# Kernel optimization log

Measured on AMD Instinct MI355X. Metric: run time of the kernel, lower is better.

Reference implementation:

```python
import jax, jax.numpy as jnp
import numpy as np

K = 50          # NEC paper uses p=50 neighbors
DELTA = 1e-3    # kernel smoothing constant


def setup_inputs() -> dict:
    key = jax.random.key(0)
    ks = jax.random.split(key, 8)
    B, D_IN, D, A, C = 512, 2, 128, 3, 200000
    s = lambda fan_in: 1.0 / np.sqrt(fan_in)
    return {
        "x": jax.random.normal(ks[0], (B, D_IN), jnp.float32),
        "W1": jax.random.normal(ks[1], (D_IN, D), jnp.float32) * s(D_IN),
        "b1": jnp.zeros((D,), jnp.float32),
        "W2": jax.random.normal(ks[2], (D, D), jnp.float32) * s(D),
        "b2": jnp.zeros((D,), jnp.float32),
        "W3": jax.random.normal(ks[3], (D, D), jnp.float32) * s(D),
        "b3": jnp.zeros((D,), jnp.float32),
        "W4": jax.random.normal(ks[4], (D, D), jnp.float32) * s(D),
        "b4": jnp.zeros((D,), jnp.float32),
        "keys": jax.random.normal(ks[5], (A, C, D), jnp.float32),
        "mem_values": jax.random.normal(ks[6], (A, C), jnp.float32),
    }


def _encode(x, W1, b1, W2, b2, W3, b3, W4, b4):
    h = jax.nn.relu(x @ W1 + b1)
    h = jax.nn.relu(h @ W2 + b2)
    h = jax.nn.relu(h @ W3 + b3)
    return h @ W4 + b4  # [B, D]


def _dnd_lookup(h, keys, mem_values):
    # h: [B, D]; keys: [A, C, D]; mem_values: [A, C]
    q2 = jnp.sum(h * h, axis=-1)                       # [B]
    k2 = jnp.sum(keys * keys, axis=-1)                 # [A, C]
    cross = jnp.einsum("bd,acd->bac", h, keys)         # [B, A, C]
    d2 = jnp.maximum(q2[:, None, None] + k2[None] - 2.0 * cross, 0.0)
    neg_d, idx = jax.lax.top_k(-d2, K)                  # [B, A, K]
    d_top = -neg_d
    w = 1.0 / (d_top + DELTA)                           # NEC kernel
    w = w / jnp.sum(w, axis=-1, keepdims=True)
    a_idx = jnp.arange(keys.shape[0])[None, :, None]    # [1, A, 1]
    v_top = mem_values[a_idx, idx]                      # gather -> [B, A, K]
    values = jnp.sum(w * v_top, axis=-1)                # [B, A]
    return values


def reference(x, W1, b1, W2, b2, W3, b3, W4, b4, keys, mem_values):
    h = _encode(x, W1, b1, W2, b2, W3, b3, W4, b4)
    values = _dnd_lookup(h, keys, mem_values)
    actions = jnp.argmax(values, axis=-1)
    return values, actions
```

## Files before the change

kernel.cpp:

```cpp
#include <hip/hip_runtime.h>
#include <hip/hip_bf16.h>
#include <math.h>

#define B_    512
#define DIM   128
#define A_    3
#define C_    200000
#define K_    50
#define DELTA 1e-3

typedef __attribute__((ext_vector_type(8))) short bf16x8;
typedef __attribute__((ext_vector_type(4))) float f32x4;

#define NBIN_A 128
#define CAP_A  1024
#define ROWCH  12500

#define NBLK4  250
#define GT4    32
#define GTPB4  25

#define AOFF_H64   0u
#define AOFF_H32   524288u
#define AOFF_HBF   786432u
#define AOFF_Q2    917504u
#define AOFF_V64   1718272u
#define AOFF_BINS  8022016u
#define NEED_A     (8022016ull + 307200000ull)

#define NBIN_B 192
#define CAP_B  768
#define BM_B   64
#define BN_B   128
#define TPC_B  16
#define CHUNK_B (TPC_B*BN_B)
#define NCH_B  ((C_ + CHUNK_B - 1)/CHUNK_B)

#define BOFF_H32   0u
#define BOFF_H64   262144u
#define BOFF_Q2    786432u
#define BOFF_K2    788480u
#define BOFF_HIST  3188480u
#define BOFF_TAU   4368128u
#define BOFF_CNT   4374272u
#define BOFF_V64   4380416u
#define BOFF_CAND  4392704u

static __device__ inline unsigned short f2bf(float x) {
    union { float f; unsigned u; } c; c.f = x;
    unsigned r = (c.u + 0x7FFFu + ((c.u >> 16) & 1u)) >> 16;
    return (unsigned short)r;
}
static __device__ inline unsigned pkbf(float a, float b) {
    __hip_bfloat162 t = __float22bfloat162_rn(make_float2(a, b));
    union { __hip_bfloat162 h; unsigned u; } cv; cv.h = t; return cv.u;
}

__global__ __launch_bounds__(128) void mlp_kernel(
    const float* __restrict__ x,
    const float* __restrict__ W1, const float* __restrict__ b1,
    const float* __restrict__ W2, const float* __restrict__ b2,
    const float* __restrict__ W3, const float* __restrict__ b3,
    const float* __restrict__ W4, const float* __restrict__ b4,
    float* __restrict__ h32, unsigned short* __restrict__ hbf,
    double* __restrict__ h64, float* __restrict__ q2)
{
    int b = blockIdx.x, t = threadIdx.x;
    __shared__ double s0[DIM], s1[DIM];
    double x0 = (double)x[b*2+0], x1 = (double)x[b*2+1];
    double h = x0*(double)W1[t] + x1*(double)W1[DIM+t] + (double)b1[t];
    s0[t] = h > 0.0 ? h : 0.0;
    __syncthreads();
    double acc = (double)b2[t];
    for (int k = 0; k < DIM; k++) acc += s0[k]*(double)W2[k*DIM+t];
    s1[t] = acc > 0.0 ? acc : 0.0;
    __syncthreads();
    acc = (double)b3[t];
    for (int k = 0; k < DIM; k++) acc += s1[k]*(double)W3[k*DIM+t];
    s0[t] = acc > 0.0 ? acc : 0.0;
    __syncthreads();
    acc = (double)b4[t];
    for (int k = 0; k < DIM; k++) acc += s0[k]*(double)W4[k*DIM+t];
    h64[b*DIM+t] = acc;
    float hf = (float)acc;
    h32[b*DIM+t] = hf;
    hbf[b*DIM+t] = f2bf(hf);
    s1[t] = acc*acc;
    __syncthreads();
    for (int s = 64; s > 0; s >>= 1) { if (t < s) s1[t] += s1[t+s]; __syncthreads(); }
    if (t == 0) q2[b] = (float)s1[0];
}

static __device__ inline void load2(float4 lv[2], const float* __restrict__ ka,
                                    int nrow, int hh) {
    const float4* gp = (const float4*)(ka + (size_t)nrow*DIM) + hh*2;
    lv[0] = gp[0]; lv[1] = gp[1];
}
static __device__ inline void conv_store32(const float4 lv[2], char* sBn,
                                           float* k2n, int r, int hh) {
    float4 v0 = lv[0], v1 = lv[1];
    float ss = v0.x*v0.x + v0.y*v0.y + v0.z*v0.z + v0.w*v0.w
             + v1.x*v1.x + v1.y*v1.y + v1.z*v1.z + v1.w*v1.w;
    int4 pk;
    pk.x = (int)pkbf(v0.x, v0.y); pk.y = (int)pkbf(v0.z, v0.w);
    pk.z = (int)pkbf(v1.x, v1.y); pk.w = (int)pkbf(v1.z, v1.w);
    *(int4*)(sBn + r*256 + ((hh ^ (r & 7)) << 4)) = pk;
    ss += __shfl_xor(ss, 1, 64);
    ss += __shfl_xor(ss, 2, 64);
    ss += __shfl_xor(ss, 4, 64);
    ss += __shfl_xor(ss, 8, 64);
    if (hh == 0) k2n[r] = ss;
}

__global__ __launch_bounds__(512, 1) void gemm4_kernel(
    const float* __restrict__ keys, const unsigned short* __restrict__ hbf,
    const float* __restrict__ q2, unsigned char* __restrict__ bins)
{
    const int blk = blockIdx.x, a = blockIdx.y;
    const int tid = threadIdx.x;
    const int lane = tid & 63, w = tid >> 6;
    const int lm = lane & 15, kh = lane >> 4;

    __shared__ __align__(16) short sA[512*128];
    __shared__ __align__(16) short sB[2][32*128];
    __shared__ float q2s[512];
    __shared__ float k2s[2][32];

    #pragma unroll
    for (int u = 0; u < 16; u++) {
        int idx = u*512 + tid;
        int rr = idx >> 4, cc = idx & 15;
        int4 gv = ((const int4*)hbf)[rr*16 + cc];
        *(int4*)((char*)sA + rr*256 + ((cc ^ (rr & 7)) << 4)) = gv;
    }
    q2s[tid] = q2[tid];

    const int r = tid >> 4, hh = tid & 15;
    const float* ka = keys + (size_t)a*C_*DIM;
    const int nbase = blk*(GT4*GTPB4);

    float4 lv[2];
    load2(lv, ka, nbase + r, hh);
    conv_store32(lv, (char*)&sB[0][0], k2s[0], r, hh);
    __syncthreads();

    unsigned char* rp0; unsigned char* rp1; unsigned char* rp2; unsigned char* rp3;
    {
        unsigned char* base = bins + (size_t)(a*B_)*C_ + kh*4;
        rp0 = base + (size_t)(w*64 +  0 + lm)*C_;
        rp1 = base + (size_t)(w*64 + 16 + lm)*C_;
        rp2 = base + (size_t)(w*64 + 32 + lm)*C_;
        rp3 = base + (size_t)(w*64 + 48 + lm)*C_;
    }

    unsigned pkp[8];
    #pragma unroll
    for (int u = 0; u < 8; u++) pkp[u] = 0;
    int n0_prev = 0;

    int cur = 0;
    for (int t = 0; t < GTPB4; t++) {
        const int n0 = nbase + t*GT4;
        const bool more = (t + 1 < GTPB4);

        if (more) load2(lv, ka, n0 + GT4 + r, hh);
        if (t > 0) {
            *(unsigned*)(rp0 + n0_prev     ) = pkp[0];
            *(unsigned*)(rp0 + n0_prev + 16) = pkp[1];
            *(unsigned*)(rp1 + n0_prev     ) = pkp[2];
            *(unsigned*)(rp1 + n0_prev + 16) = pkp[3];
            *(unsigned*)(rp2 + n0_prev     ) = pkp[4];
            *(unsigned*)(rp2 + n0_prev + 16) = pkp[5];
            *(unsigned*)(rp3 + n0_prev     ) = pkp[6];
            *(unsigned*)(rp3 + n0_prev + 16) = pkp[7];
        }

        f32x4 acc[2][4];
        #pragma unroll
        for (int i = 0; i < 2; i++)
            #pragma unroll
            for (int j = 0; j < 4; j++) acc[i][j] = (f32x4){0.f, 0.f, 0.f, 0.f};

        const char* sBc = (const char*)&sB[cur][0];
        #pragma unroll
        for (int kst = 0; kst < 4; kst++) {
            bf16x8 af[2], bfv[4];
            #pragma unroll
            for (int i = 0; i < 2; i++) {
                int nr = i*16 + lm;
                af[i] = *(const bf16x8*)(sBc + nr*256 + ((((kst<<2) + kh) ^ (nr & 7)) << 4));
            }
            #pragma unroll
            for (int j = 0; j < 4; j++) {
                int br = w*64 + j*16 + lm;
                bfv[j] = *(const bf16x8*)((const char*)sA + br*256 + ((((kst<<2) + kh) ^ (br & 7)) << 4));
            }
            #pragma unroll
            for (int i = 0; i < 2; i++)
                #pragma unroll
                for (int j = 0; j < 4; j++)
                    acc[i][j] = __builtin_amdgcn_mfma_f32_16x16x32_bf16(af[i], bfv[j], acc[i][j], 0, 0, 0);
        }

        {
            float4 kq0 = *(const float4*)&k2s[cur][kh*4];
            float4 kq1 = *(const float4*)&k2s[cur][16 + kh*4];
            #pragma unroll
            for (int j = 0; j < 4; j++) {
                float q2v = q2s[w*64 + j*16 + lm];
                #pragma unroll
                for (int i = 0; i < 2; i++) {
                    float4 kq = (i == 0) ? kq0 : kq1;
                    unsigned pk = 0;
                    #pragma unroll
                    for (int rg = 0; rg < 4; rg++) {
                        float kv = (rg == 0) ? kq.x : (rg == 1) ? kq.y : (rg == 2) ? kq.z : kq.w;
                        float d2v = (q2v + kv) - 2.0f*acc[i][j][rg];
                        float dc = fminf(fmaxf(d2v, 16.0f), 4095.0f);
                        unsigned bin = (__float_as_uint(dc) >> 19) - 2096u;
                        pk |= bin << (8*rg);
                    }
                    pkp[j*2 + i] = pk;
                }
            }
            n0_prev = n0;
        }

        if (more) conv_store32(lv, (char*)&sB[cur ^ 1][0], k2s[cur ^ 1], r, hh);
        __syncthreads();
        cur ^= 1;
    }
    *(unsigned*)(rp0 + n0_prev     ) = pkp[0];
    *(unsigned*)(rp0 + n0_prev + 16) = pkp[1];
    *(unsigned*)(rp1 + n0_prev     ) = pkp[2];
    *(unsigned*)(rp1 + n0_prev + 16) = pkp[3];
    *(unsigned*)(rp2 + n0_prev     ) = pkp[4];
    *(unsigned*)(rp2 + n0_prev + 16) = pkp[5];
    *(unsigned*)(rp3 + n0_prev     ) = pkp[6];
    *(unsigned*)(rp3 + n0_prev + 16) = pkp[7];
}

__global__ __launch_bounds__(512) void finish_kernel(
    const unsigned char* __restrict__ bins, const float* __restrict__ keys,
    const double* __restrict__ h64, const float* __restrict__ mem_values,
    float* __restrict__ out_values, double* __restrict__ val64)
{
    const int q = blockIdx.x;
    const int a = q >> 9, b = q & 511;
    const int p = b*A_ + a;
    const int tid = threadIdx.x;

    __shared__ unsigned hist_s[NBIN_A*32];
    __shared__ unsigned hc[NBIN_A];
    __shared__ double hd[DIM];
    __shared__ int    cidx[CAP_A];
    __shared__ double d2s[CAP_A];
    __shared__ float  vs[CAP_A];
    __shared__ double redv[8];
    __shared__ int    redi8[8];
    __shared__ double acc_w, acc_wv;
    __shared__ unsigned cnt_s;
    __shared__ int thr_s;

    for (int i = tid; i < NBIN_A*32; i += 512) hist_s[i] = 0;
    for (int i = tid; i < DIM; i += 512) hd[i] = h64[(size_t)b*DIM + i];
    if (tid == 0) { cnt_s = 0; acc_w = 0.0; acc_wv = 0.0; }
    __syncthreads();

    const uint4* row = (const uint4*)(bins + (size_t)q*C_);
    const int rep = tid & 31;
    for (int ch = tid; ch < ROWCH; ch += 512) {
        uint4 v = row[ch];
        unsigned d[4] = {v.x, v.y, v.z, v.w};
        #pragma unroll
        for (int e = 0; e < 4; e++) {
            unsigned x = d[e];
            atomicAdd(&hist_s[((x      ) & 127u)*32 + rep], 1u);
            atomicAdd(&hist_s[((x >>  8) & 127u)*32 + rep], 1u);
            atomicAdd(&hist_s[((x >> 16) & 127u)*32 + rep], 1u);
            atomicAdd(&hist_s[((x >> 24) & 127u)*32 + rep], 1u);
        }
    }
    __syncthreads();
    if (tid < NBIN_A) {
        unsigned s = 0;
        #pragma unroll
        for (int r2 = 0; r2 < 32; r2++) s += hist_s[tid*32 + r2];
        hc[tid] = s;
    }
    __syncthreads();
    if (tid == 0) {
        unsigned cum = 0; int jsel = NBIN_A-1;
        for (int j = 0; j < NBIN_A; j++) { cum += hc[j]; if (cum >= K_) { jsel = j; break; } }
        unsigned c1 = cum + (jsel+1 < NBIN_A ? hc[jsel+1] : 0u);
        unsigned c2 = c1  + (jsel+2 < NBIN_A ? hc[jsel+2] : 0u);
        int jt = (c2 <= 768u) ? jsel+2 : jsel+1;
        if (jt > NBIN_A-1) jt = NBIN_A-1;
        thr_s = jt + 1;
    }
    __syncthreads();
    const unsigned thr  = (unsigned)thr_s;
    const unsigned addv = (128u - thr) * 0x01010101u;
    for (int ch = tid; ch < ROWCH; ch += 512) {
        uint4 v = row[ch];
        unsigned d[4] = {v.x, v.y, v.z, v.w};
        #pragma unroll
        for (int e = 0; e < 4; e++) {
            unsigned m = (d[e] + addv) & 0x80808080u;
            if (m != 0x80808080u) {
                #pragma unroll
                for (int by = 0; by < 4; by++) {
                    if (!((m >> (8*by + 7)) & 1u)) {
                        unsigned pos = atomicAdd(&cnt_s, 1u);
                        if (pos < CAP_A) cidx[pos] = ch*16 + e*4 + by;
                    }
                }
            }
        }
    }
    __syncthreads();
    int n = (int)cnt_s; if (n > CAP_A) n = CAP_A;

    for (int i = tid; i < n; i += 512) {
        int c = cidx[i];
        const float4* kr = (const float4*)(keys + ((size_t)a*C_ + c)*DIM);
        double s0 = 0.0, s1 = 0.0;
        #pragma unroll 4
        for (int kq = 0; kq < 32; kq++) {
            float4 kv = kr[kq];
            double d0 = hd[4*kq+0] - (double)kv.x;
            double d1 = hd[4*kq+1] - (double)kv.y;
            double d2 = hd[4*kq+2] - (double)kv.z;
            double d3 = hd[4*kq+3] - (double)kv.w;
            s0 += d0*d0 + d1*d1; s1 += d2*d2 + d3*d3;
        }
        d2s[i] = s0 + s1;
        vs[i]  = mem_values[(size_t)a*C_ + c];
    }
    __syncthreads();

    int kk = n < K_ ? n : K_;
    for (int t = 0; t < kk; t++) {
        double best = 1e300; int bi = -1;
        for (int i = tid; i < n; i += 512)
            if (d2s[i] < best) { best = d2s[i]; bi = i; }
        #pragma unroll
        for (int off = 32; off > 0; off >>= 1) {
            double ov = __shfl_xor(best, off, 64);
            int    oi = __shfl_xor(bi,   off, 64);
            if (ov < best) { best = ov; bi = oi; }
        }
        int wv = tid >> 6;
        if ((tid & 63) == 0) { redv[wv] = best; redi8[wv] = bi; }
        __syncthreads();
        if (tid == 0) {
            double bv = redv[0]; int wi = redi8[0];
            #pragma unroll
            for (int u = 1; u < 8; u++)
                if (redv[u] < bv) { bv = redv[u]; wi = redi8[u]; }
            double d = d2s[wi]; if (d < 0.0) d = 0.0;
            double wgt = 1.0 / (d + DELTA);
            acc_w += wgt; acc_wv += wgt * (double)vs[wi];
            d2s[wi] = 2e300;
        }
        __syncthreads();
    }
    if (tid == 0) {
        double v = acc_wv / acc_w;
        out_values[p] = (float)v;
        val64[p] = v;
    }
}

__global__ __launch_bounds__(256) void k2_kernel(const float* __restrict__ keys,
                                                 float* __restrict__ k2)
{
    int r = blockIdx.x*4 + (threadIdx.x >> 6);
    int lane = threadIdx.x & 63;
    float2 v = ((const float2*)keys)[(size_t)r*64 + lane];
    float s = v.x*v.x + v.y*v.y;
    #pragma unroll
    for (int off = 32; off > 0; off >>= 1) s += __shfl_down(s, off, 64);
    if (lane == 0) k2[r] = s;
}

template<int MODE>
__global__ __launch_bounds__(256) void pass_kernel(
    const float* __restrict__ keys, const float* __restrict__ h32,
    const float* __restrict__ q2,   const float* __restrict__ k2,
    unsigned* __restrict__ hist,    const float* __restrict__ tau,
    unsigned* __restrict__ cnt,     int* __restrict__ cand)
{
    const int bt = blockIdx.x;
    const int ch = blockIdx.y;
    const int a  = blockIdx.z;
    const int b0 = bt*BM_B;
    const int tid = threadIdx.x;
    const int tx = tid & 31, ty = tid >> 5;

    __shared__ float4 hs4[BM_B*33];
    __shared__ float4 ks4[BN_B*33];
    __shared__ float  q2s[BM_B];
    __shared__ float  taus[BM_B];
    __shared__ unsigned hist_s[MODE == 0 ? BM_B*NBIN_B : 1];

    #pragma unroll
    for (int q = 0; q < BM_B*32/256; q++) {
        int flat = q*256 + tid; int row = flat >> 5, kq = flat & 31;
        hs4[row*33 + kq] = ((const float4*)h32)[(size_t)(b0+row)*32 + kq];
    }
    if (tid < BM_B) {
        q2s[tid] = q2[b0+tid];
        if (MODE == 1) taus[tid] = tau[(b0+tid)*A_ + a];
    }
    if (MODE == 0) for (int i = tid; i < BM_B*NBIN_B; i += 256) hist_s[i] = 0;
    const float* __restrict__ k2g = k2 + (size_t)a*C_;

    for (int t = 0; t < TPC_B; t++) {
        int n0 = ch*CHUNK_B + t*BN_B;
        if (n0 >= C_) break;
        __syncthreads();
        #pragma unroll
        for (int q = 0; q < 16; q++) {
            int flat = q*256 + tid; int row = flat >> 5, kq = flat & 31;
            int nr = n0 + row; if (nr >= C_) nr = C_-1;
            ks4[row*33 + kq] = ((const float4*)keys)[((size_t)a*C_ + nr)*32 + kq];
        }
        __syncthreads();

        float acc[8][4];
        #pragma unroll
        for (int i = 0; i < 8; i++)
            #pragma unroll
            for (int j = 0; j < 4; j++) acc[i][j] = 0.0f;

        for (int kq = 0; kq < 32; kq++) {
            float4 hv[8], kv[4];
            #pragma unroll
            for (int i = 0; i < 8; i++) hv[i] = hs4[(ty*8+i)*33 + kq];
            #pragma unroll
            for (int j = 0; j < 4; j++) kv[j] = ks4[(j*32+tx)*33 + kq];
            #pragma unroll
            for (int i = 0; i < 8; i++)
                #pragma unroll
                for (int j = 0; j < 4; j++)
                    acc[i][j] += hv[i].x*kv[j].x + hv[i].y*kv[j].y
                               + hv[i].z*kv[j].z + hv[i].w*kv[j].w;
        }

        #pragma unroll
        for (int i = 0; i < 8; i++) {
            int bl = ty*8 + i;
            float q2b = q2s[bl];
            #pragma unroll
            for (int j = 0; j < 4; j++) {
                int n = n0 + j*32 + tx;
                if (n < C_) {
                    float d2f = fmaxf(q2b + k2g[n] - 2.0f*acc[i][j], 0.0f);
                    if (MODE == 0) {
                        int bin = (int)(__float_as_uint(d2f + 1.0f) >> 19) - 2032;
                        bin = bin < 0 ? 0 : (bin > NBIN_B-1 ? NBIN_B-1 : bin);
                        atomicAdd(&hist_s[bl*NBIN_B + bin], 1u);
                    } else {
                        if (d2f < taus[bl]) {
                            int p = (b0+bl)*A_ + a;
                            unsigned pos = atomicAdd(&cnt[p], 1u);
                            if (pos < CAP_B) cand[(size_t)p*CAP_B + pos] = n;
                        }
                    }
                }
            }
        }
    }
    if (MODE == 0) {
        __syncthreads();
        for (int i = tid; i < BM_B*NBIN_B; i += 256) {
            unsigned v = hist_s[i];
            if (v) {
                int bl = i / NBIN_B, bin = i % NBIN_B;
                atomicAdd(&hist[(size_t)((b0+bl)*A_ + a)*NBIN_B + bin], v);
            }
        }
    }
}

__global__ __launch_bounds__(256) void tauB_kernel(const unsigned* __restrict__ hist,
                                                   float* __restrict__ tau)
{
    int p = blockIdx.x*256 + threadIdx.x;
    if (p >= B_*A_) return;
    const unsigned* hp = hist + (size_t)p*NBIN_B;
    unsigned cum = 0; int jsel = NBIN_B-1;
    for (int j = 0; j < NBIN_B; j++) { cum += hp[j]; if (cum >= K_) { jsel = j; break; } }
    tau[p] = __uint_as_float((unsigned)(2034 + jsel) << 19) - 1.0f;
}

__global__ __launch_bounds__(256) void select_kernel(
    const float* __restrict__ keys, const double* __restrict__ h64,
    const float* __restrict__ mem_values,
    const unsigned* __restrict__ cnt, const int* __restrict__ cand,
    float* __restrict__ out_values, double* __restrict__ val64, int cap)
{
    int p = blockIdx.x; int b = p / A_, a = p % A_;
    int tid = threadIdx.x;
    __shared__ double hd[DIM];
    __shared__ double d2s[CAP_A];
    __shared__ float  vs[CAP_A];
    __shared__ double redv[4];
    __shared__ int    redi4[4];
    __shared__ double acc_w, acc_wv;

    for (int i = tid; i < DIM; i += 256) hd[i] = h64[(size_t)b*DIM + i];
    if (tid == 0) { acc_w = 0.0; acc_wv = 0.0; }
    __syncthreads();

    int n = (int)cnt[p]; if (n > cap) n = cap;
    for (int i = tid; i < n; i += 256) {
        int c = cand[(size_t)p*cap + i];
        const float4* kr = (const float4*)(keys + ((size_t)a*C_ + c)*DIM);
        double s0 = 0.0, s1 = 0.0;
        #pragma unroll 4
        for (int kq = 0; kq < 32; kq++) {
            float4 kv = kr[kq];
            double d0 = hd[4*kq+0] - (double)kv.x;
            double d1 = hd[4*kq+1] - (double)kv.y;
            double d2 = hd[4*kq+2] - (double)kv.z;
            double d3 = hd[4*kq+3] - (double)kv.w;
            s0 += d0*d0 + d1*d1; s1 += d2*d2 + d3*d3;
        }
        d2s[i] = s0 + s1;
        vs[i]  = mem_values[(size_t)a*C_ + c];
    }
    __syncthreads();

    int kk = n < K_ ? n : K_;
    for (int t = 0; t < kk; t++) {
        double best = 1e300; int bi = -1;
        for (int i = tid; i < n; i += 256)
            if (d2s[i] < best) { best = d2s[i]; bi = i; }
        #pragma unroll
        for (int off = 32; off > 0; off >>= 1) {
            double ov = __shfl_xor(best, off, 64);
            int    oi = __shfl_xor(bi,   off, 64);
            if (ov < best) { best = ov; bi = oi; }
        }
        int wv = tid >> 6;
        if ((tid & 63) == 0) { redv[wv] = best; redi4[wv] = bi; }
        __syncthreads();
        if (tid == 0) {
            double bv = redv[0]; int wi = redi4[0];
            if (redv[1] < bv) { bv = redv[1]; wi = redi4[1]; }
            if (redv[2] < bv) { bv = redv[2]; wi = redi4[2]; }
            if (redv[3] < bv) { bv = redv[3]; wi = redi4[3]; }
            double d = d2s[wi]; if (d < 0.0) d = 0.0;
            double wgt = 1.0 / (d + DELTA);
            acc_w += wgt; acc_wv += wgt * (double)vs[wi];
            d2s[wi] = 2e300;
        }
        __syncthreads();
    }
    if (tid == 0) {
        double v = acc_wv / acc_w;
        out_values[p] = (float)v;
        val64[p] = v;
    }
}

__global__ void argmax_kernel(const double* __restrict__ val64, float* __restrict__ out)
{
    int b = blockIdx.x*blockDim.x + threadIdx.x;
    if (b >= B_) return;
    double v0 = val64[b*A_+0], v1 = val64[b*A_+1], v2 = val64[b*A_+2];
    int bi = 0; double bv = v0;
    if (v1 > bv) { bv = v1; bi = 1; }
    if (v2 > bv) { bv = v2; bi = 2; }
    out[B_*A_ + b] = (float)bi;
}

extern "C" void kernel_launch(void* const* d_in, const int* in_sizes, int n_in,
                              void* d_out, int out_size, void* d_ws, size_t ws_size,
                              hipStream_t stream)
{
    const float* x    = (const float*)d_in[0];
    const float* W1   = (const float*)d_in[1];
    const float* b1   = (const float*)d_in[2];
    const float* W2   = (const float*)d_in[3];
    const float* b2   = (const float*)d_in[4];
    const float* W3   = (const float*)d_in[5];
    const float* b3   = (const float*)d_in[6];
    const float* W4   = (const float*)d_in[7];
    const float* b4   = (const float*)d_in[8];
    const float* keys = (const float*)d_in[9];
    const float* memv = (const float*)d_in[10];

    char* ws = (char*)d_ws;

    if (ws_size >= NEED_A) {
        double*         h64  = (double*)        (ws + AOFF_H64);
        float*          h32  = (float*)         (ws + AOFF_H32);
        unsigned short* hbf  = (unsigned short*)(ws + AOFF_HBF);
        float*          q2   = (float*)         (ws + AOFF_Q2);
        double*         v64  = (double*)        (ws + AOFF_V64);
        unsigned char*  bins = (unsigned char*) (ws + AOFF_BINS);

        mlp_kernel<<<B_, 128, 0, stream>>>(x, W1, b1, W2, b2, W3, b3, W4, b4, h32, hbf, h64, q2);
        gemm4_kernel<<<dim3(NBLK4, A_), 512, 0, stream>>>(keys, hbf, q2, bins);
        finish_kernel<<<B_*A_, 512, 0, stream>>>(bins, keys, h64, memv, (float*)d_out, v64);
        argmax_kernel<<<2, 256, 0, stream>>>(v64, (float*)d_out);
    } else {
        float*          h32  = (float*)         (ws + BOFF_H32);
        double*         h64  = (double*)        (ws + BOFF_H64);
        float*          q2   = (float*)         (ws + BOFF_Q2);
        float*          k2   = (float*)         (ws + BOFF_K2);
        unsigned*       hist = (unsigned*)      (ws + BOFF_HIST);
        float*          tau  = (float*)         (ws + BOFF_TAU);
        unsigned*       cnt  = (unsigned*)      (ws + BOFF_CNT);
        double*         v64  = (double*)        (ws + BOFF_V64);
        int*            cand = (int*)           (ws + BOFF_CAND);
        unsigned short* hbf  = (unsigned short*)(ws + BOFF_CAND);

        hipMemsetAsync(ws + BOFF_HIST, 0, (BOFF_CNT + B_*A_*4) - BOFF_HIST, stream);

        mlp_kernel<<<B_, 128, 0, stream>>>(x, W1, b1, W2, b2, W3, b3, W4, b4, h32, hbf, h64, q2);
        k2_kernel<<<(A_*C_)/4, 256, 0, stream>>>(keys, k2);
        pass_kernel<0><<<dim3(B_/BM_B, NCH_B, A_), 256, 0, stream>>>(keys, h32, q2, k2, hist, nullptr, nullptr, nullptr);
        tauB_kernel<<<(B_*A_ + 255)/256, 256, 0, stream>>>(hist, tau);
        pass_kernel<1><<<dim3(B_/BM_B, NCH_B, A_), 256, 0, stream>>>(keys, h32, q2, k2, nullptr, tau, cnt, cand);
        select_kernel<<<B_*A_, 256, 0, stream>>>(keys, h64, memv, cnt, cand, (float*)d_out, v64, CAP_B);
        argmax_kernel<<<2, 256, 0, stream>>>(v64, (float*)d_out);
    }
}
```

Baseline: 966.6 us.

## Add per-32-key group minimum bins to skip scanning far groups in finish

The GEMM kernel now also records, for each query and each group of 32 keys, the minimum distance bin, written to a compact per-query array. The finish kernel first builds a coarse histogram over these group minima to bound the needed bin window. It then scans only the groups whose minimum falls within that window, for both the histogram pass and the candidate collection pass. This avoids reading the full 200000-byte bin row twice per query. The cost is extra shuffles and scattered byte stores in the GEMM, plus more workspace.

```diff
diff --git a/kernel.cpp b/kernel.cpp
--- a/kernel.cpp
+++ b/kernel.cpp
@@ -14,11 +14,12 @@
 
 #define NBIN_A 128
 #define CAP_A  1024
-#define ROWCH  12500
 
 #define NBLK4  250
 #define GT4    32
 #define GTPB4  25
+#define NGRP   6250
+#define MINC_STR 6272
 
 #define AOFF_H64   0u
 #define AOFF_H32   524288u
@@ -26,7 +27,8 @@
 #define AOFF_Q2    917504u
 #define AOFF_V64   1718272u
 #define AOFF_BINS  8022016u
-#define NEED_A     (8022016ull + 307200000ull)
+#define AOFF_MINC  315222016ull
+#define NEED_A     (315222016ull + 9633792ull)
 
 #define NBIN_B 192
 #define CAP_B  768
@@ -114,7 +116,8 @@
 
 __global__ __launch_bounds__(512, 1) void gemm4_kernel(
     const float* __restrict__ keys, const unsigned short* __restrict__ hbf,
-    const float* __restrict__ q2, unsigned char* __restrict__ bins)
+    const float* __restrict__ q2, unsigned char* __restrict__ bins,
+    unsigned char* __restrict__ minc)
 {
     const int blk = blockIdx.x, a = blockIdx.y;
     const int tid = threadIdx.x;
@@ -205,9 +208,11 @@
         {
             float4 kq0 = *(const float4*)&k2s[cur][kh*4];
             float4 kq1 = *(const float4*)&k2s[cur][16 + kh*4];
+            const int g = blk*GTPB4 + t;
             #pragma unroll
             for (int j = 0; j < 4; j++) {
                 float q2v = q2s[w*64 + j*16 + lm];
+                unsigned mn = 255u;
                 #pragma unroll
                 for (int i = 0; i < 2; i++) {
                     float4 kq = (i == 0) ? kq0 : kq1;
@@ -219,9 +224,14 @@
                         float dc = fminf(fmaxf(d2v, 16.0f), 4095.0f);
                         unsigned bin = (__float_as_uint(dc) >> 19) - 2096u;
                         pk |= bin << (8*rg);
+                        mn = bin < mn ? bin : mn;
                     }
                     pkp[j*2 + i] = pk;
                 }
+                unsigned m1 = __shfl_xor(mn, 16, 64); mn = m1 < mn ? m1 : mn;
+                unsigned m2 = __shfl_xor(mn, 32, 64); mn = m2 < mn ? m2 : mn;
+                if (kh == 0)
+                    minc[(size_t)(a*B_ + w*64 + j*16 + lm)*MINC_STR + g] = (unsigned char)mn;
             }
             n0_prev = n0;
         }
@@ -241,7 +251,8 @@
 }
 
 __global__ __launch_bounds__(512) void finish_kernel(
-    const unsigned char* __restrict__ bins, const float* __restrict__ keys,
+    const unsigned char* __restrict__ bins, const unsigned char* __restrict__ minc,
+    const float* __restrict__ keys,
     const double* __restrict__ h64, const float* __restrict__ mem_values,
     float* __restrict__ out_values, double* __restrict__ val64)
 {
@@ -253,6 +264,7 @@
     __shared__ unsigned hist_s[NBIN_A*32];
     __shared__ unsigned hc[NBIN_A];
     __shared__ double hd[DIM];
+    __shared__ unsigned char minb_s[MINC_STR];
     __shared__ int    cidx[CAP_A];
     __shared__ double d2s[CAP_A];
     __shared__ float  vs[CAP_A];
@@ -260,25 +272,65 @@
     __shared__ int    redi8[8];
     __shared__ double acc_w, acc_wv;
     __shared__ unsigned cnt_s;
-    __shared__ int thr_s;
+    __shared__ int thr_s, W_s;
 
     for (int i = tid; i < NBIN_A*32; i += 512) hist_s[i] = 0;
     for (int i = tid; i < DIM; i += 512) hd[i] = h64[(size_t)b*DIM + i];
     if (tid == 0) { cnt_s = 0; acc_w = 0.0; acc_wv = 0.0; }
     __syncthreads();
 
-    const uint4* row = (const uint4*)(bins + (size_t)q*C_);
     const int rep = tid & 31;
-    for (int ch = tid; ch < ROWCH; ch += 512) {
-        uint4 v = row[ch];
+
+    if (tid < MINC_STR/16) {
+        const uint4* mrow = (const uint4*)(minc + (size_t)q*MINC_STR);
+        uint4 v = mrow[tid];
+        if (tid == 390) { v.z |= 0xFFFF0000u; v.w = 0xFFFFFFFFu; }
+        if (tid == 391) { v.x = v.y = v.z = v.w = 0xFFFFFFFFu; }
+        ((uint4*)minb_s)[tid] = v;
         unsigned d[4] = {v.x, v.y, v.z, v.w};
         #pragma unroll
         for (int e = 0; e < 4; e++) {
             unsigned x = d[e];
-            atomicAdd(&hist_s[((x      ) & 127u)*32 + rep], 1u);
-            atomicAdd(&hist_s[((x >>  8) & 127u)*32 + rep], 1u);
-            atomicAdd(&hist_s[((x >> 16) & 127u)*32 + rep], 1u);
-            atomicAdd(&hist_s[((x >> 24) & 127u)*32 + rep], 1u);
+            #pragma unroll
+            for (int by = 0; by < 4; by++) {
+                unsigned bb = (x >> (8*by)) & 255u;
+                if (bb < 128u) atomicAdd(&hist_s[bb*32 + rep], 1u);
+            }
+        }
+    }
+    __syncthreads();
+    if (tid < NBIN_A) {
+        unsigned s = 0;
+        #pragma unroll
+        for (int r2 = 0; r2 < 32; r2++) s += hist_s[tid*32 + r2];
+        hc[tid] = s;
+    }
+    __syncthreads();
+    if (tid == 0) {
+        unsigned cum = 0; int jhi = NBIN_A-1;
+        for (int j = 0; j < NBIN_A; j++) { cum += hc[j]; if (cum >= K_) { jhi = j; break; } }
+        int Wv = jhi + 2; if (Wv > NBIN_A-1) Wv = NBIN_A-1;
+        W_s = Wv;
+    }
+    __syncthreads();
+    const int W = W_s;
+
+    for (int i = tid; i < NBIN_A*32; i += 512) hist_s[i] = 0;
+    __syncthreads();
+
+    const uint4* row = (const uint4*)(bins + (size_t)q*C_);
+    for (int g = tid; g < NGRP; g += 512) {
+        if ((int)minb_s[g] <= W) {
+            uint4 v0 = row[2*g], v1 = row[2*g+1];
+            unsigned d[8] = {v0.x, v0.y, v0.z, v0.w, v1.x, v1.y, v1.z, v1.w};
+            #pragma unroll
+            for (int e = 0; e < 8; e++) {
+                unsigned x = d[e];
+                atomicAdd(&hist_s[((x      ) & 127u)*32 + rep], 1u);
+                atomicAdd(&hist_s[((x >>  8) & 127u)*32 + rep], 1u);
+                atomicAdd(&hist_s[((x >> 16) & 127u)*32 + rep], 1u);
+                atomicAdd(&hist_s[((x >> 24) & 127u)*32 + rep], 1u);
+            }
         }
     }
     __syncthreads();
@@ -301,18 +353,21 @@
     __syncthreads();
     const unsigned thr  = (unsigned)thr_s;
     const unsigned addv = (128u - thr) * 0x01010101u;
-    for (int ch = tid; ch < ROWCH; ch += 512) {
-        uint4 v = row[ch];
-        unsigned d[4] = {v.x, v.y, v.z, v.w};
-        #pragma unroll
-        for (int e = 0; e < 4; e++) {
-            unsigned m = (d[e] + addv) & 0x80808080u;
-            if (m != 0x80808080u) {
-                #pragma unroll
-                for (int by = 0; by < 4; by++) {
-                    if (!((m >> (8*by + 7)) & 1u)) {
-                        unsigned pos = atomicAdd(&cnt_s, 1u);
-                        if (pos < CAP_A) cidx[pos] = ch*16 + e*4 + by;
+
+    for (int g = tid; g < NGRP; g += 512) {
+        if ((unsigned)minb_s[g] < thr) {
+            uint4 v0 = row[2*g], v1 = row[2*g+1];
+            unsigned d[8] = {v0.x, v0.y, v0.z, v0.w, v1.x, v1.y, v1.z, v1.w};
+            #pragma unroll
+            for (int e = 0; e < 8; e++) {
+                unsigned m = (d[e] + addv) & 0x80808080u;
+                if (m != 0x80808080u) {
+                    #pragma unroll
+                    for (int by = 0; by < 4; by++) {
+                        if (!((m >> (8*by + 7)) & 1u)) {
+                            unsigned pos = atomicAdd(&cnt_s, 1u);
+                            if (pos < CAP_A) cidx[pos] = g*32 + e*4 + by;
+                        }
                     }
                 }
             }
@@ -602,10 +657,11 @@
         float*          q2   = (float*)         (ws + AOFF_Q2);
         double*         v64  = (double*)        (ws + AOFF_V64);
         unsigned char*  bins = (unsigned char*) (ws + AOFF_BINS);
+        unsigned char*  minc = (unsigned char*) (ws + AOFF_MINC);
 
         mlp_kernel<<<B_, 128, 0, stream>>>(x, W1, b1, W2, b2, W3, b3, W4, b4, h32, hbf, h64, q2);
-        gemm4_kernel<<<dim3(NBLK4, A_), 512, 0, stream>>>(keys, hbf, q2, bins);
-        finish_kernel<<<B_*A_, 512, 0, stream>>>(bins, keys, h64, memv, (float*)d_out, v64);
+        gemm4_kernel<<<dim3(NBLK4, A_), 512, 0, stream>>>(keys, hbf, q2, bins, minc);
+        finish_kernel<<<B_*A_, 512, 0, stream>>>(bins, minc, keys, h64, memv, (float*)d_out, v64);
         argmax_kernel<<<2, 256, 0, stream>>>(v64, (float*)d_out);
     } else {
         float*          h32  = (float*)         (ws + BOFF_H32);
```

Result: slower. 986.7 us (+2.1%).
